# Kernel tuning notes

Measured on AMD Instinct MI355X. Metric: run time of the kernel, lower is better.

Reference implementation:

```python
import jax, jax.numpy as jnp
import numpy as np

N_NODES = 100000
DIM = 4
N_EDGES = 3200000


def setup_inputs() -> dict:
    key = jax.random.key(0)
    k1, k2, k3 = jax.random.split(key, 3)
    x = jax.random.normal(k1, (N_NODES, DIM), dtype=jnp.float32)
    edge_index = jax.random.randint(k2, (2, N_EDGES), 0, N_NODES, dtype=jnp.int64)
    boo_values = jax.random.normal(k3, (N_EDGES, DIM, DIM), dtype=jnp.float32)
    return {"x": x, "edge_index": edge_index, "boo_values": boo_values}


def _spmv(x, edge_index, A):
    # y_i = sum_j A_{ij} x_j ; edge e = (row=edge_index[0], col=edge_index[1])
    # PyG flow='target_to_source': gather x at col, scatter-add at row.
    row, col = edge_index[0], edge_index[1]
    msg = jnp.einsum('eij,ej->ei', A, x[col])  # [E, dim]
    return jax.ops.segment_sum(msg, row, num_segments=x.shape[0])


def _spmv_t(x, edge_index, A):
    # y_j = sum_i A_{ij}^T x_i ; flow='source_to_target': gather at row, scatter at col.
    row, col = edge_index[0], edge_index[1]
    msg = jnp.einsum('eji,ej->ei', A, x[row])  # A^T matvec, [E, dim]
    return jax.ops.segment_sum(msg, col, num_segments=x.shape[0])


def reference(x, edge_index, boo_values):
    lt_x = _spmv_t(x, edge_index, boo_values)   # L^T x
    return _spmv(lt_x, edge_index, boo_values)  # L (L^T x)
```

## Files before the change

kernel.cpp:

```cpp
#include <hip/hip_runtime.h>

static constexpr int N_NODES = 100000;
static constexpr int N_EDGES = 3200000;
static constexpr int NBK    = 26;
static constexpr int NPB    = 3848;
static constexpr int SLOTS  = NBK * NPB;
static constexpr int WGC    = 1024;
static constexpr int CHUNK  = N_EDGES / WGC;
static constexpr int PSPLIT = 20;


__global__ void __launch_bounds__(256) k_count(
    const int* __restrict__ row, const int* __restrict__ col,
    unsigned* __restrict__ cmC, unsigned* __restrict__ cmR)
{
    __shared__ unsigned hC[NBK], hR[NBK];
    if (threadIdx.x < NBK) { hC[threadIdx.x] = 0u; hR[threadIdx.x] = 0u; }
    __syncthreads();
    int w = blockIdx.x, e0 = w * CHUNK;
    for (int e = e0 + threadIdx.x; e < e0 + CHUNK; e += 256) {
        atomicAdd(&hC[col[e] / NPB], 1u);
        atomicAdd(&hR[row[e] / NPB], 1u);
    }
    __syncthreads();
    if (threadIdx.x < NBK) {
        cmC[(size_t)threadIdx.x * WGC + w] = hC[threadIdx.x];
        cmR[(size_t)threadIdx.x * WGC + w] = hR[threadIdx.x];
    }
}

__global__ void __launch_bounds__(256) k_prefix(
    unsigned* __restrict__ cmC, unsigned* __restrict__ cmR,
    unsigned* __restrict__ totC, unsigned* __restrict__ totR)
{
    int warp = (blockIdx.x * 256 + threadIdx.x) >> 6;
    int lane = threadIdx.x & 63;
    if (warp >= 2 * NBK) return;
    unsigned* cm  = (warp < NBK) ? cmC : cmR;
    unsigned* tot = (warp < NBK) ? totC : totR;
    int b = (warp < NBK) ? warp : warp - NBK;
    unsigned* rowp = cm + (size_t)b * WGC;
    unsigned carry = 0;
    for (int base = 0; base < WGC; base += 64) {
        unsigned v = rowp[base + lane];
        unsigned inc = v;
        for (int off = 1; off < 64; off <<= 1) {
            unsigned t = __shfl_up(inc, off, 64);
            if (lane >= off) inc += t;
        }
        rowp[base + lane] = carry + inc - v;
        carry += __shfl(inc, 63, 64);
    }
    if (lane == 0) tot[b] = carry;
}

__global__ void __launch_bounds__(64) k_scan(
    const unsigned* __restrict__ totC, const unsigned* __restrict__ totR,
    unsigned* __restrict__ baseC, unsigned* __restrict__ baseR)
{
    if (threadIdx.x == 0) {
        unsigned s = 0;
        for (int b = 0; b < NBK; ++b) { baseC[b] = s; s += totC[b]; }
    } else if (threadIdx.x == 1) {
        unsigned s = 0;
        for (int b = 0; b < NBK; ++b) { baseR[b] = s; s += totR[b]; }
    }
}

__global__ void __launch_bounds__(256) k_part(
    const int* __restrict__ key,
    const int* __restrict__ pay,
    const unsigned* __restrict__ cm,
    const unsigned* __restrict__ base,
    uint2* __restrict__ perm)
{
    __shared__ uint2 stage[CHUNK];
    __shared__ unsigned hist[NBK];
    __shared__ unsigned runstart[NBK + 1];
    __shared__ unsigned gdst[NBK];
    int w = blockIdx.x, tid = threadIdx.x, e0 = w * CHUNK;

    if (tid < NBK) {
        hist[tid] = 0u;
        gdst[tid] = base[tid] + cm[(size_t)tid * WGC + w];
    }
    __syncthreads();
    for (int e = e0 + tid; e < e0 + CHUNK; e += 256)
        atomicAdd(&hist[key[e] / NPB], 1u);
    __syncthreads();
    if (tid == 0) {
        unsigned s = 0;
        for (int b = 0; b < NBK; ++b) { runstart[b] = s; s += hist[b]; }
        runstart[NBK] = s;
    }
    __syncthreads();
    if (tid < NBK) hist[tid] = runstart[tid];
    __syncthreads();
    for (int e = e0 + tid; e < e0 + CHUNK; e += 256) {
        int k = key[e], p = pay[e];
        int b = k / NPB;
        int loc = k - b * NPB;
        unsigned pos = atomicAdd(&hist[b], 1u);
        stage[pos] = make_uint2((unsigned)e,
                                (unsigned)p | ((unsigned)loc << 17));
    }
    __syncthreads();
    for (int s = tid; s < CHUNK; s += 256) {
        int lo = 0, hi = NBK;
        while (hi - lo > 1) {
            int mid = (lo + hi) >> 1;
            if (runstart[mid] <= (unsigned)s) lo = mid; else hi = mid;
        }
        perm[(size_t)gdst[lo] + (unsigned)s - runstart[lo]] = stage[s];
    }
}

template<int TRANS>
__global__ void __launch_bounds__(512) k_reduce(
    const uint2* __restrict__ perm,
    const float4* __restrict__ vin,
    const float4* __restrict__ boo,
    const unsigned* __restrict__ base, const unsigned* __restrict__ tot,
    float4* __restrict__ part)
{
    __shared__ float acc[4][NPB];
    int b = blockIdx.x / PSPLIT, sub = blockIdx.x % PSPLIT;
    int tid = threadIdx.x;
    for (int i = tid; i < 4 * NPB; i += 512) ((float*)acc)[i] = 0.f;
    __syncthreads();
    unsigned start = base[b], n = tot[b];
    unsigned lo = start + (unsigned)(((unsigned long long)n * sub) / PSPLIT);
    unsigned hi = start + (unsigned)(((unsigned long long)n * (sub + 1)) / PSPLIT);
    for (unsigned i = lo + tid; i < hi; i += 512) {
        uint2 rec = perm[i];
        unsigned e   = rec.x;
        unsigned src = rec.y & 0x1FFFFu;
        unsigned loc = rec.y >> 17;
        float4 v  = vin[src];
        float4 a0 = boo[(size_t)e * 4 + 0];
        float4 a1 = boo[(size_t)e * 4 + 1];
        float4 a2 = boo[(size_t)e * 4 + 2];
        float4 a3 = boo[(size_t)e * 4 + 3];
        float m0, m1, m2, m3;
        if (TRANS) {
            m0 = a0.x * v.x + a1.x * v.y + a2.x * v.z + a3.x * v.w;
            m1 = a0.y * v.x + a1.y * v.y + a2.y * v.z + a3.y * v.w;
            m2 = a0.z * v.x + a1.z * v.y + a2.z * v.z + a3.z * v.w;
            m3 = a0.w * v.x + a1.w * v.y + a2.w * v.z + a3.w * v.w;
        } else {
            m0 = a0.x * v.x + a0.y * v.y + a0.z * v.z + a0.w * v.w;
            m1 = a1.x * v.x + a1.y * v.y + a1.z * v.z + a1.w * v.w;
            m2 = a2.x * v.x + a2.y * v.y + a2.z * v.z + a2.w * v.w;
            m3 = a3.x * v.x + a3.y * v.y + a3.z * v.z + a3.w * v.w;
        }
        atomicAdd(&acc[0][loc], m0);
        atomicAdd(&acc[1][loc], m1);
        atomicAdd(&acc[2][loc], m2);
        atomicAdd(&acc[3][loc], m3);
    }
    __syncthreads();
    float4* dst = part + (size_t)sub * SLOTS + (size_t)b * NPB;
    for (int i = tid; i < NPB; i += 512)
        dst[i] = make_float4(acc[0][i], acc[1][i], acc[2][i], acc[3][i]);
}

__global__ void __launch_bounds__(256) k_merge(
    const float4* __restrict__ part, float4* __restrict__ vout)
{
    int s = blockIdx.x * 256 + threadIdx.x;
    if (s >= N_NODES) return;
    float4 r = part[s];
    for (int sub = 1; sub < PSPLIT; ++sub) {
        float4 t = part[(size_t)sub * SLOTS + s];
        r.x += t.x; r.y += t.y; r.z += t.z; r.w += t.w;
    }
    vout[s] = r;
}


__global__ void __launch_bounds__(256) llt_pass1(
    const float* __restrict__ x, const int* __restrict__ row_idx,
    const int* __restrict__ col_idx, const float* __restrict__ boo,
    float* __restrict__ lt)
{
    int t = blockIdx.x * blockDim.x + threadIdx.x;
    if (t >= N_EDGES * 4) return;
    int e = t >> 2, i = t & 3;
    int r = row_idx[e], c = col_idx[e];
    const float* A = boo + (size_t)e * 16;
    const float* xv = x + (size_t)r * 4;
    float m = A[0*4+i]*xv[0] + A[1*4+i]*xv[1] + A[2*4+i]*xv[2] + A[3*4+i]*xv[3];
    atomicAdd(lt + (size_t)c * 4 + i, m);
}

__global__ void __launch_bounds__(256) llt_pass2(
    const float4* __restrict__ lt, const int* __restrict__ row_idx,
    const int* __restrict__ col_idx, const float4* __restrict__ boo,
    float* __restrict__ out)
{
    int t = blockIdx.x * blockDim.x + threadIdx.x;
    if (t >= N_EDGES * 4) return;
    int e = t >> 2, i = t & 3;
    int r = row_idx[e], c = col_idx[e];
    float4 arow = boo[(size_t)e * 4 + i];
    float4 lv = lt[c];
    float m = arow.x*lv.x + arow.y*lv.y + arow.z*lv.z + arow.w*lv.w;
    atomicAdd(out + (size_t)r * 4 + i, m);
}


extern "C" void kernel_launch(void* const* d_in, const int* in_sizes, int n_in,
                              void* d_out, int out_size, void* d_ws, size_t ws_size,
                              hipStream_t stream) {
    const float4* x = (const float4*)d_in[0];
    const int* edge_index = (const int*)d_in[1];
    const float4* boo = (const float4*)d_in[2];
    const int* row = edge_index;
    const int* col = edge_index + N_EDGES;
    float4* out = (float4*)d_out;

    auto align256 = [](size_t v) { return (v + 255) & ~(size_t)255; };
    const size_t sz_cm   = align256((size_t)NBK * WGC * 4);
    const size_t sz_vec  = align256((size_t)NBK * 4);
    const size_t sz_perm = align256((size_t)N_EDGES * 8);
    const size_t sz_lt   = align256((size_t)N_NODES * 16);
    const size_t sz_part = align256((size_t)PSPLIT * SLOTS * 16);
    const size_t need = 2 * sz_cm + 4 * sz_vec + sz_perm + sz_lt + sz_part;

    if (ws_size >= need) {
        char* p = (char*)d_ws;
        unsigned* cmC   = (unsigned*)p; p += sz_cm;
        unsigned* cmR   = (unsigned*)p; p += sz_cm;
        unsigned* totC  = (unsigned*)p; p += sz_vec;
        unsigned* totR  = (unsigned*)p; p += sz_vec;
        unsigned* baseC = (unsigned*)p; p += sz_vec;
        unsigned* baseR = (unsigned*)p; p += sz_vec;
        uint2*    perm  = (uint2*)p;    p += sz_perm;
        float4*   lt    = (float4*)p;   p += sz_lt;
        float4*   part  = (float4*)p;   p += sz_part;

        k_count<<<WGC, 256, 0, stream>>>(row, col, cmC, cmR);
        k_prefix<<<(2 * NBK * 64 + 255) / 256, 256, 0, stream>>>(cmC, cmR, totC, totR);
        k_scan<<<1, 64, 0, stream>>>(totC, totR, baseC, baseR);
        k_part<<<WGC, 256, 0, stream>>>(col, row, cmC, baseC, perm);
        k_reduce<1><<<NBK * PSPLIT, 512, 0, stream>>>(perm, x, boo, baseC, totC, part);
        k_merge<<<(N_NODES + 255) / 256, 256, 0, stream>>>(part, lt);
        k_part<<<WGC, 256, 0, stream>>>(row, col, cmR, baseR, perm);
        k_reduce<0><<<NBK * PSPLIT, 512, 0, stream>>>(perm, (const float4*)lt, boo, baseR, totR, part);
        k_merge<<<(N_NODES + 255) / 256, 256, 0, stream>>>(part, out);
    } else {
        float* ltf = (float*)d_ws;
        hipMemsetAsync(ltf, 0, (size_t)N_NODES * 4 * sizeof(float), stream);
        hipMemsetAsync(out, 0, (size_t)N_NODES * 4 * sizeof(float), stream);
        const int grid = (N_EDGES * 4 + 255) / 256;
        llt_pass1<<<grid, 256, 0, stream>>>((const float*)x, row, col, (const float*)boo, ltf);
        llt_pass2<<<grid, 256, 0, stream>>>((const float4*)ltf, row, col, boo, (float*)out);
    }
}
```

Baseline: 282.1 us.

## Compute edge messages before partitioning, store them as bf16, use power-of-two buckets

Adds a k_msg kernel that computes each edge's 4-vector message in edge order, with coalesced reads of the block values. It packs the message to bf16 so that the partition and reduce kernels move compact messages instead of gathering boo and x in scattered permuted order. The buckets become power-of-two sized (1024 nodes, shift and mask instead of divide), WGC becomes 1000 and PSPLIT drops to 8. The risk is precision loss from bf16 messages, which may fail tolerance, plus extra global traffic for the msgE, msgS and locS buffers.

```diff
diff --git a/kernel.cpp b/kernel.cpp
--- a/kernel.cpp
+++ b/kernel.cpp
@@ -2,13 +2,51 @@
 
 static constexpr int N_NODES = 100000;
 static constexpr int N_EDGES = 3200000;
-static constexpr int NBK    = 26;
-static constexpr int NPB    = 3848;
+static constexpr int SHIFT  = 10;
+static constexpr int NPB    = 1 << SHIFT;
+static constexpr int NBK    = (N_NODES + NPB - 1) / NPB;
 static constexpr int SLOTS  = NBK * NPB;
-static constexpr int WGC    = 1024;
+static constexpr int WGC    = 1000;
 static constexpr int CHUNK  = N_EDGES / WGC;
-static constexpr int PSPLIT = 20;
-
+static constexpr int PSPLIT = 8;
+
+__device__ __forceinline__ unsigned bf16rne(float f) {
+    unsigned u = __float_as_uint(f);
+    u += 0x7fffu + ((u >> 16) & 1u);
+    return u >> 16;
+}
+__device__ __forceinline__ unsigned pack2(float lo, float hi) {
+    return bf16rne(lo) | (bf16rne(hi) << 16);
+}
+
+template<int TRANS>
+__global__ void __launch_bounds__(256) k_msg(
+    const int* __restrict__ pay,
+    const float4* __restrict__ vin,
+    const float4* __restrict__ boo,
+    uint2* __restrict__ msgE)
+{
+    int e = blockIdx.x * 256 + threadIdx.x;
+    if (e >= N_EDGES) return;
+    float4 v  = vin[pay[e]];
+    float4 q0 = boo[(size_t)e * 4 + 0];
+    float4 q1 = boo[(size_t)e * 4 + 1];
+    float4 q2 = boo[(size_t)e * 4 + 2];
+    float4 q3 = boo[(size_t)e * 4 + 3];
+    float m0, m1, m2, m3;
+    if (TRANS) {
+        m0 = q0.x * v.x + q1.x * v.y + q2.x * v.z + q3.x * v.w;
+        m1 = q0.y * v.x + q1.y * v.y + q2.y * v.z + q3.y * v.w;
+        m2 = q0.z * v.x + q1.z * v.y + q2.z * v.z + q3.z * v.w;
+        m3 = q0.w * v.x + q1.w * v.y + q2.w * v.z + q3.w * v.w;
+    } else {
+        m0 = q0.x * v.x + q0.y * v.y + q0.z * v.z + q0.w * v.w;
+        m1 = q1.x * v.x + q1.y * v.y + q1.z * v.z + q1.w * v.w;
+        m2 = q2.x * v.x + q2.y * v.y + q2.z * v.z + q2.w * v.w;
+        m3 = q3.x * v.x + q3.y * v.y + q3.z * v.z + q3.w * v.w;
+    }
+    msgE[e] = make_uint2(pack2(m0, m1), pack2(m2, m3));
+}
 
 __global__ void __launch_bounds__(256) k_count(
     const int* __restrict__ row, const int* __restrict__ col,
@@ -19,8 +57,8 @@
     __syncthreads();
     int w = blockIdx.x, e0 = w * CHUNK;
     for (int e = e0 + threadIdx.x; e < e0 + CHUNK; e += 256) {
-        atomicAdd(&hC[col[e] / NPB], 1u);
-        atomicAdd(&hR[row[e] / NPB], 1u);
+        atomicAdd(&hC[col[e] >> SHIFT], 1u);
+        atomicAdd(&hR[row[e] >> SHIFT], 1u);
     }
     __syncthreads();
     if (threadIdx.x < NBK) {
@@ -42,13 +80,14 @@
     unsigned* rowp = cm + (size_t)b * WGC;
     unsigned carry = 0;
     for (int base = 0; base < WGC; base += 64) {
-        unsigned v = rowp[base + lane];
+        int idx = base + lane;
+        unsigned v = (idx < WGC) ? rowp[idx] : 0u;
         unsigned inc = v;
         for (int off = 1; off < 64; off <<= 1) {
             unsigned t = __shfl_up(inc, off, 64);
             if (lane >= off) inc += t;
         }
-        rowp[base + lane] = carry + inc - v;
+        if (idx < WGC) rowp[idx] = carry + inc - v;
         carry += __shfl(inc, 63, 64);
     }
     if (lane == 0) tot[b] = carry;
@@ -69,12 +108,14 @@
 
 __global__ void __launch_bounds__(256) k_part(
     const int* __restrict__ key,
-    const int* __restrict__ pay,
+    const uint2* __restrict__ msgE,
     const unsigned* __restrict__ cm,
     const unsigned* __restrict__ base,
-    uint2* __restrict__ perm)
-{
-    __shared__ uint2 stage[CHUNK];
+    uint2* __restrict__ msgS,
+    unsigned* __restrict__ locS)
+{
+    __shared__ uint2 smsg[CHUNK];
+    __shared__ unsigned short sloc[CHUNK];
     __shared__ unsigned hist[NBK];
     __shared__ unsigned runstart[NBK + 1];
     __shared__ unsigned gdst[NBK];
@@ -86,7 +127,7 @@
     }
     __syncthreads();
     for (int e = e0 + tid; e < e0 + CHUNK; e += 256)
-        atomicAdd(&hist[key[e] / NPB], 1u);
+        atomicAdd(&hist[key[e] >> SHIFT], 1u);
     __syncthreads();
     if (tid == 0) {
         unsigned s = 0;
@@ -96,30 +137,30 @@
     __syncthreads();
     if (tid < NBK) hist[tid] = runstart[tid];
     __syncthreads();
+
     for (int e = e0 + tid; e < e0 + CHUNK; e += 256) {
-        int k = key[e], p = pay[e];
-        int b = k / NPB;
-        int loc = k - b * NPB;
+        int k = key[e];
+        int b = k >> SHIFT;
         unsigned pos = atomicAdd(&hist[b], 1u);
-        stage[pos] = make_uint2((unsigned)e,
-                                (unsigned)p | ((unsigned)loc << 17));
-    }
-    __syncthreads();
+        smsg[pos] = msgE[e];
+        sloc[pos] = (unsigned short)(k & (NPB - 1));
+    }
+    __syncthreads();
+
     for (int s = tid; s < CHUNK; s += 256) {
         int lo = 0, hi = NBK;
         while (hi - lo > 1) {
             int mid = (lo + hi) >> 1;
             if (runstart[mid] <= (unsigned)s) lo = mid; else hi = mid;
         }
-        perm[(size_t)gdst[lo] + (unsigned)s - runstart[lo]] = stage[s];
-    }
-}
-
-template<int TRANS>
+        size_t g = (size_t)gdst[lo] + (unsigned)s - runstart[lo];
+        msgS[g] = smsg[s];
+        locS[g] = (unsigned)sloc[s];
+    }
+}
+
 __global__ void __launch_bounds__(512) k_reduce(
-    const uint2* __restrict__ perm,
-    const float4* __restrict__ vin,
-    const float4* __restrict__ boo,
+    const uint2* __restrict__ msgS, const unsigned* __restrict__ locS,
     const unsigned* __restrict__ base, const unsigned* __restrict__ tot,
     float4* __restrict__ part)
 {
@@ -132,31 +173,12 @@
     unsigned lo = start + (unsigned)(((unsigned long long)n * sub) / PSPLIT);
     unsigned hi = start + (unsigned)(((unsigned long long)n * (sub + 1)) / PSPLIT);
     for (unsigned i = lo + tid; i < hi; i += 512) {
-        uint2 rec = perm[i];
-        unsigned e   = rec.x;
-        unsigned src = rec.y & 0x1FFFFu;
-        unsigned loc = rec.y >> 17;
-        float4 v  = vin[src];
-        float4 a0 = boo[(size_t)e * 4 + 0];
-        float4 a1 = boo[(size_t)e * 4 + 1];
-        float4 a2 = boo[(size_t)e * 4 + 2];
-        float4 a3 = boo[(size_t)e * 4 + 3];
-        float m0, m1, m2, m3;
-        if (TRANS) {
-            m0 = a0.x * v.x + a1.x * v.y + a2.x * v.z + a3.x * v.w;
-            m1 = a0.y * v.x + a1.y * v.y + a2.y * v.z + a3.y * v.w;
-            m2 = a0.z * v.x + a1.z * v.y + a2.z * v.z + a3.z * v.w;
-            m3 = a0.w * v.x + a1.w * v.y + a2.w * v.z + a3.w * v.w;
-        } else {
-            m0 = a0.x * v.x + a0.y * v.y + a0.z * v.z + a0.w * v.w;
-            m1 = a1.x * v.x + a1.y * v.y + a1.z * v.z + a1.w * v.w;
-            m2 = a2.x * v.x + a2.y * v.y + a2.z * v.z + a2.w * v.w;
-            m3 = a3.x * v.x + a3.y * v.y + a3.z * v.z + a3.w * v.w;
-        }
-        atomicAdd(&acc[0][loc], m0);
-        atomicAdd(&acc[1][loc], m1);
-        atomicAdd(&acc[2][loc], m2);
-        atomicAdd(&acc[3][loc], m3);
+        uint2 m = msgS[i];
+        int loc = (int)locS[i];
+        atomicAdd(&acc[0][loc], __uint_as_float(m.x << 16));
+        atomicAdd(&acc[1][loc], __uint_as_float(m.x & 0xffff0000u));
+        atomicAdd(&acc[2][loc], __uint_as_float(m.y << 16));
+        atomicAdd(&acc[3][loc], __uint_as_float(m.y & 0xffff0000u));
     }
     __syncthreads();
     float4* dst = part + (size_t)sub * SLOTS + (size_t)b * NPB;
@@ -222,10 +244,13 @@
     auto align256 = [](size_t v) { return (v + 255) & ~(size_t)255; };
     const size_t sz_cm   = align256((size_t)NBK * WGC * 4);
     const size_t sz_vec  = align256((size_t)NBK * 4);
-    const size_t sz_perm = align256((size_t)N_EDGES * 8);
+    const size_t sz_msgE = align256((size_t)N_EDGES * 8);
+    const size_t sz_msgS = align256((size_t)N_EDGES * 8);
+    const size_t sz_loc  = align256((size_t)N_EDGES * 4);
     const size_t sz_lt   = align256((size_t)N_NODES * 16);
     const size_t sz_part = align256((size_t)PSPLIT * SLOTS * 16);
-    const size_t need = 2 * sz_cm + 4 * sz_vec + sz_perm + sz_lt + sz_part;
+    const size_t need = 2 * sz_cm + 4 * sz_vec + sz_msgE + sz_msgS + sz_loc
+                      + sz_lt + sz_part;
 
     if (ws_size >= need) {
         char* p = (char*)d_ws;
@@ -235,18 +260,24 @@
         unsigned* totR  = (unsigned*)p; p += sz_vec;
         unsigned* baseC = (unsigned*)p; p += sz_vec;
         unsigned* baseR = (unsigned*)p; p += sz_vec;
-        uint2*    perm  = (uint2*)p;    p += sz_perm;
+        uint2*    msgE  = (uint2*)p;    p += sz_msgE;
+        uint2*    msgS  = (uint2*)p;    p += sz_msgS;
+        unsigned* locS  = (unsigned*)p; p += sz_loc;
         float4*   lt    = (float4*)p;   p += sz_lt;
         float4*   part  = (float4*)p;   p += sz_part;
+
+        const int mgrid = (N_EDGES + 255) / 256;
 
         k_count<<<WGC, 256, 0, stream>>>(row, col, cmC, cmR);
         k_prefix<<<(2 * NBK * 64 + 255) / 256, 256, 0, stream>>>(cmC, cmR, totC, totR);
         k_scan<<<1, 64, 0, stream>>>(totC, totR, baseC, baseR);
-        k_part<<<WGC, 256, 0, stream>>>(col, row, cmC, baseC, perm);
-        k_reduce<1><<<NBK * PSPLIT, 512, 0, stream>>>(perm, x, boo, baseC, totC, part);
+        k_msg<1><<<mgrid, 256, 0, stream>>>(row, x, boo, msgE);
+        k_part<<<WGC, 256, 0, stream>>>(col, msgE, cmC, baseC, msgS, locS);
+        k_reduce<<<NBK * PSPLIT, 512, 0, stream>>>(msgS, locS, baseC, totC, part);
         k_merge<<<(N_NODES + 255) / 256, 256, 0, stream>>>(part, lt);
-        k_part<<<WGC, 256, 0, stream>>>(row, col, cmR, baseR, perm);
-        k_reduce<0><<<NBK * PSPLIT, 512, 0, stream>>>(perm, (const float4*)lt, boo, baseR, totR, part);
+        k_msg<0><<<mgrid, 256, 0, stream>>>(col, (const float4*)lt, boo, msgE);
+        k_part<<<WGC, 256, 0, stream>>>(row, msgE, cmR, baseR, msgS, locS);
+        k_reduce<<<NBK * PSPLIT, 512, 0, stream>>>(msgS, locS, baseR, totR, part);
         k_merge<<<(N_NODES + 255) / 256, 256, 0, stream>>>(part, out);
     } else {
         float* ltf = (float*)d_ws;
```

New measurement: 362.7 us. +28.5%, slower.
